# Kernel tuning notes

Hardware: AMD Instinct MI355X
Metric: run time of the kernel (lower is better)

The kernel has to match this reference:

```python
import jax, jax.numpy as jnp
from jax import lax
import numpy as np

N, CIN, COUT, H, W = 8, 64, 64, 256, 256
KH = KW = 3
AUX, HID = 128, 256


def setup_inputs() -> dict:
    key = jax.random.key(0)
    ks = jax.random.split(key, 12)
    k = float(np.sqrt(1.0 / (CIN * KH * KW)))
    inp = {
        "x": jax.random.normal(ks[0], (N, CIN, H, W), jnp.float32),
        "y": jax.random.normal(ks[1], (N, AUX), jnp.float32),
        "weight": jax.random.uniform(ks[2], (COUT, CIN, KH, KW), jnp.float32, -k, k),
        # modulation MLP: Linear(AUX->HID), PReLU, Linear(HID->COUT*CIN), Sigmoid
        "fc_w1": jax.random.normal(ks[3], (HID, AUX), jnp.float32) * 0.05,
        "fc_b1": jax.random.normal(ks[4], (HID,), jnp.float32) * 0.05,
        "fc_prelu": jnp.asarray(0.25, jnp.float32),
        "fc_w2": jax.random.normal(ks[5], (COUT * CIN, HID), jnp.float32) * 0.05,
        "fc_b2": jax.random.normal(ks[6], (COUT * CIN,), jnp.float32) * 0.05,
        # learned-bias MLP: Linear(AUX->HID), PReLU, Linear(HID->COUT)
        "bias_w1": jax.random.normal(ks[7], (HID, AUX), jnp.float32) * 0.05,
        "bias_b1": jax.random.normal(ks[8], (HID,), jnp.float32) * 0.05,
        "bias_prelu": jnp.asarray(0.25, jnp.float32),
        "bias_w2": jax.random.normal(ks[9], (COUT, HID), jnp.float32) * 0.05,
        "bias_b2": jax.random.normal(ks[10], (COUT,), jnp.float32) * 0.05,
    }
    return inp


def _prelu(h, a):
    return jnp.where(h >= 0, h, a * h)


def reference(x, y, weight, fc_w1, fc_b1, fc_prelu, fc_w2, fc_b2,
              bias_w1, bias_b1, bias_prelu, bias_w2, bias_b2):
    n, cin, h_, w_ = x.shape
    cout = weight.shape[0]
    # modulation factors: (N, COUT*CIN), sigmoid activation
    hm = _prelu(y @ fc_w1.T + fc_b1, fc_prelu)
    mod = jax.nn.sigmoid(hm @ fc_w2.T + fc_b2)
    # per-sample modulated kernels: (N, COUT, CIN, KH, KW)
    w_mod = mod.reshape(n, cout, cin, 1, 1) * weight
    # grouped conv with groups = batch, expressed as vmap over batch
    def conv1(xi, wi):  # xi: (CIN,H,W), wi: (COUT,CIN,KH,KW)
        return lax.conv_general_dilated(
            xi[None], wi, window_strides=(1, 1), padding=[(1, 1), (1, 1)],
            rhs_dilation=(1, 1))[0]
    out = jax.vmap(conv1)(x, w_mod)  # (N, COUT, H, W)
    # learned per-sample bias
    hb = _prelu(y @ bias_w1.T + bias_b1, bias_prelu)
    b = hb @ bias_w2.T + bias_b2  # (N, COUT)
    return out + b[:, :, None, None]
```

## Files before the change

kernel.cpp:

```cpp
#include <hip/hip_runtime.h>
#include <hip/hip_bf16.h>


typedef short bf16x8 __attribute__((ext_vector_type(8)));
typedef float f32x16 __attribute__((ext_vector_type(16)));

#define NB 8
#define CIN 64
#define COUT 64
#define HH 256
#define WW 256
#define HWP (HH * WW)
#define AUXD 128
#define HIDD 256

#define XH 4128
#define XRW (2 * XH)
#define XBUF (4 * XRW)
#define WOFF (2 * XBUF)
#define WBYTES (9 * 8 * 64 * 16)
#define SMEMB (WOFF + WBYTES)

__device__ __forceinline__ unsigned short f2bf(float f) {
    unsigned u = __builtin_bit_cast(unsigned, f);
    u += 0x7FFFu + ((u >> 16) & 1u);
    return (unsigned short)(u >> 16);
}

__device__ __forceinline__ unsigned pk2(float a, float b, float vm) {
    return (unsigned)f2bf(a * vm) | ((unsigned)f2bf(b * vm) << 16);
}

__global__ __launch_bounds__(256) void mlp_kernel(
    const float* __restrict__ y, const float* __restrict__ weight,
    const float* __restrict__ fc_w1, const float* __restrict__ fc_b1,
    const float* __restrict__ fc_prelu,
    const float* __restrict__ fc_w2, const float* __restrict__ fc_b2,
    const float* __restrict__ bias_w1, const float* __restrict__ bias_b1,
    const float* __restrict__ bias_prelu,
    const float* __restrict__ bias_w2, const float* __restrict__ bias_b2,
    unsigned short* __restrict__ w_bf, float* __restrict__ bvec)
{
    const int n = blockIdx.y;
    const int c = blockIdx.x;
    const int tid = threadIdx.x;
    __shared__ float ylds[AUXD];
    __shared__ float hl[HIDD];
    if (tid < AUXD) ylds[tid] = y[n * AUXD + tid];
    __syncthreads();

    if (c < 16) {
        float s = fc_b1[tid];
        const float* wrow = fc_w1 + tid * AUXD;
        #pragma unroll 4
        for (int a = 0; a < AUXD; ++a) s += ylds[a] * wrow[a];
        float ap = fc_prelu[0];
        hl[tid] = s >= 0.f ? s : ap * s;
        __syncthreads();

        int o = c * 256 + tid;
        float t = fc_b2[o];
        const float* w2row = fc_w2 + o * HIDD;
        #pragma unroll 4
        for (int h = 0; h < HIDD; ++h) t += hl[h] * w2row[h];
        float mod = 1.f / (1.f + expf(-t));
        int cout = o >> 6, ci = o & 63;
        int cb = ci >> 3, cl = ci & 7;
        #pragma unroll
        for (int k = 0; k < 9; ++k) {
            float wv = weight[o * 9 + k];
            w_bf[((((n * 9 + k) * 8 + cb) * 64 + cout) << 3) + cl] = f2bf(mod * wv);
        }
    } else {
        float s = bias_b1[tid];
        const float* wrow = bias_w1 + tid * AUXD;
        #pragma unroll 4
        for (int a = 0; a < AUXD; ++a) s += ylds[a] * wrow[a];
        float ap = bias_prelu[0];
        hl[tid] = s >= 0.f ? s : ap * s;
        __syncthreads();
        if (tid < COUT) {
            float t = bias_b2[tid];
            const float* w2row = bias_w2 + tid * HIDD;
            #pragma unroll 4
            for (int h = 0; h < HIDD; ++h) t += hl[h] * w2row[h];
            bvec[n * COUT + tid] = t;
        }
    }
}

#define ISSUE(k) { _Pragma("unroll") \
    for (int i = 0; i < 16; ++i) st[i] = xr[k][(size_t)(nci + i) * HWP]; }

#define WRITE(k) { float vm = vmr[k]; \
    unsigned char* dst = nx + (rg + 2 * (k)) * XRW + (sw + 1) * 16; \
    uint4 lo, hi; \
    lo.x = pk2(st[0], st[1], vm);  lo.y = pk2(st[2], st[3], vm); \
    lo.z = pk2(st[4], st[5], vm);  lo.w = pk2(st[6], st[7], vm); \
    hi.x = pk2(st[8], st[9], vm);  hi.y = pk2(st[10], st[11], vm); \
    hi.z = pk2(st[12], st[13], vm); hi.w = pk2(st[14], st[15], vm); \
    *(uint4*)dst = lo; *(uint4*)(dst + XH) = hi; }

__global__ __launch_bounds__(512, 2) void conv_kernel(
    const float* __restrict__ x, const unsigned short* __restrict__ w_bf,
    const float* __restrict__ bvec, float* __restrict__ out)
{
    __shared__ __align__(16) unsigned char smem[SMEMB];

    const int bid = blockIdx.x;
    const int n = bid & 7;
    const int h0 = (bid >> 3) * 2;

    const int tid = threadIdx.x;
    const int lane = tid & 63;
    const int wave = tid >> 6;
    const int wr = wave >> 2;
    const int wq = wave & 3;
    const int l5 = lane >> 5;
    const int l31 = lane & 31;

    const int sw = tid & 255;
    const int rg = tid >> 8;

    const float* xr[2];
    float vmr[2];
    #pragma unroll
    for (int k = 0; k < 2; ++k) {
        int r = rg + 2 * k;
        int hin = h0 - 1 + r;
        bool val = (hin >= 0) && (hin < HH);
        xr[k] = x + (size_t)n * CIN * HWP + (size_t)(val ? hin : 0) * WW + sw;
        vmr[k] = val ? 1.f : 0.f;
    }

    {
        const uint4* wsrc = (const uint4*)w_bf + (size_t)n * (9 * 8 * 64);
        #pragma unroll
        for (int it = 0; it < 9; ++it) {
            int idx = it * 512 + tid;
            uint4 v = wsrc[idx];
            *(uint4*)(smem + WOFF + (idx << 4)) = v;
        }
    }

    if (tid < 32) {
        int buf = tid >> 4, side = (tid >> 3) & 1, r = (tid >> 1) & 3, hf = tid & 1;
        uint4 z; z.x = z.y = z.z = z.w = 0u;
        *(uint4*)(smem + buf * XBUF + r * XRW + hf * XH + (side ? 257 : 0) * 16) = z;
    }

    #pragma unroll
    for (int k = 0; k < 2; ++k) {
        float st[16];
        #pragma unroll
        for (int i = 0; i < 16; ++i) st[i] = xr[k][(size_t)i * HWP];
        float vm = vmr[k];
        unsigned char* dst = smem + (rg + 2 * k) * XRW + (sw + 1) * 16;
        uint4 lo, hi;
        lo.x = pk2(st[0], st[1], vm);  lo.y = pk2(st[2], st[3], vm);
        lo.z = pk2(st[4], st[5], vm);  lo.w = pk2(st[6], st[7], vm);
        hi.x = pk2(st[8], st[9], vm);  hi.y = pk2(st[10], st[11], vm);
        hi.z = pk2(st[12], st[13], vm); hi.w = pk2(st[14], st[15], vm);
        *(uint4*)dst = lo; *(uint4*)(dst + XH) = hi;
    }

    f32x16 acc[2][2];
    #pragma unroll
    for (int m = 0; m < 2; ++m) {
        #pragma unroll
        for (int reg = 0; reg < 16; ++reg)
            acc[m][0][reg] = bvec[n * COUT + m * 32 + (reg & 3) + 8 * (reg >> 2) + 4 * l5];
        acc[m][1] = acc[m][0];
    }

    __syncthreads();

    for (int c = 0; c < 4; ++c) {
        const int p = c & 1;
        const unsigned char* rbuf = smem + p * XBUF;
        unsigned char* nx = smem + (p ^ 1) * XBUF;
        const bool more = (c < 3);
        const int nci = (c + 1) * 16;

        float st[16];
        if (more) ISSUE(0);

        #pragma unroll
        for (int kidx = 0; kidx < 9; ++kidx) {
            const int kh = kidx / 3, kw = kidx % 3;
            const unsigned char* ab = smem + WOFF +
                (((kidx * 8 + c * 2 + l5) * 64 + l31) << 4);
            bf16x8 aA = *(const bf16x8*)ab;
            bf16x8 aB = *(const bf16x8*)(ab + 512);
            const unsigned char* bb = rbuf + (wr + kh) * XRW + l5 * XH;
            bf16x8 b0 = *(const bf16x8*)(bb + (wq * 64 + l31 + kw) * 16);
            bf16x8 b1 = *(const bf16x8*)(bb + (wq * 64 + 32 + l31 + kw) * 16);

            if (more) {
                if (kidx == 3)      { WRITE(0); ISSUE(1); }
                else if (kidx == 7) { WRITE(1); }
            }

            acc[0][0] = __builtin_amdgcn_mfma_f32_32x32x16_bf16(aA, b0, acc[0][0], 0, 0, 0);
            acc[0][1] = __builtin_amdgcn_mfma_f32_32x32x16_bf16(aA, b1, acc[0][1], 0, 0, 0);
            acc[1][0] = __builtin_amdgcn_mfma_f32_32x32x16_bf16(aB, b0, acc[1][0], 0, 0, 0);
            acc[1][1] = __builtin_amdgcn_mfma_f32_32x32x16_bf16(aB, b1, acc[1][1], 0, 0, 0);
        }
        __syncthreads();
    }

    const int hout = h0 + wr;
    float* ob = out + ((size_t)n * COUT * HH + hout) * WW;
    #pragma unroll
    for (int m = 0; m < 2; ++m) {
        #pragma unroll
        for (int j = 0; j < 2; ++j) {
            int colb = wq * 64 + j * 32 + l31;
            #pragma unroll
            for (int reg = 0; reg < 16; ++reg) {
                int cout = m * 32 + (reg & 3) + 8 * (reg >> 2) + 4 * l5;
                ob[(size_t)cout * HWP + colb] = acc[m][j][reg];
            }
        }
    }
}

extern "C" void kernel_launch(void* const* d_in, const int* in_sizes, int n_in,
                              void* d_out, int out_size, void* d_ws, size_t ws_size,
                              hipStream_t stream) {
    const float* x          = (const float*)d_in[0];
    const float* y          = (const float*)d_in[1];
    const float* weight     = (const float*)d_in[2];
    const float* fc_w1      = (const float*)d_in[3];
    const float* fc_b1      = (const float*)d_in[4];
    const float* fc_prelu   = (const float*)d_in[5];
    const float* fc_w2      = (const float*)d_in[6];
    const float* fc_b2      = (const float*)d_in[7];
    const float* bias_w1    = (const float*)d_in[8];
    const float* bias_b1    = (const float*)d_in[9];
    const float* bias_prelu = (const float*)d_in[10];
    const float* bias_w2    = (const float*)d_in[11];
    const float* bias_b2    = (const float*)d_in[12];
    float* out = (float*)d_out;

    unsigned short* w_bf = (unsigned short*)d_ws;
    float* bvec = (float*)((char*)d_ws + (size_t)NB * 9 * 64 * 64 * 2);

    hipLaunchKernelGGL(mlp_kernel, dim3(17, 8), dim3(256), 0, stream,
                       y, weight, fc_w1, fc_b1, fc_prelu, fc_w2, fc_b2,
                       bias_w1, bias_b1, bias_prelu, bias_w2, bias_b2, w_bf, bvec);
    hipLaunchKernelGGL(conv_kernel, dim3(1024), dim3(512), 0, stream,
                       x, w_bf, bvec, out);
}
```

Baseline: 87.65 us.

## Double conv block to 1024 threads with one column tile per wave

Each conv block now runs 16 waves instead of 8. Every wave computes a single 32-column tile instead of two, and every thread stages one input row instead of two. The global-to-LDS prefetch schedule is rewritten so the next channel chunk is written at kidx 6 and the one after is issued at kidx 7. The goal is more waves in flight per CU to hide global-load and LDS latency in this bandwidth-heavy conv, since the large LDS footprint already allows only one block per CU. The cost is that A-operand LDS reads are duplicated across twice as many waves, and each wave does fewer MFMAs per loaded A fragment.

```diff
diff --git a/kernel.cpp b/kernel.cpp
--- a/kernel.cpp
+++ b/kernel.cpp
@@ -89,11 +89,11 @@
     }
 }
 
-#define ISSUE(k) { _Pragma("unroll") \
-    for (int i = 0; i < 16; ++i) st[i] = xr[k][(size_t)(nci + i) * HWP]; }
-
-#define WRITE(k) { float vm = vmr[k]; \
-    unsigned char* dst = nx + (rg + 2 * (k)) * XRW + (sw + 1) * 16; \
+#define ISSUE(ci0) { _Pragma("unroll") \
+    for (int i = 0; i < 16; ++i) st[i] = xrow[(size_t)((ci0) + i) * HWP]; }
+
+#define WRITE(buf) { \
+    unsigned char* dst = (buf) + rg * XRW + (sw + 1) * 16; \
     uint4 lo, hi; \
     lo.x = pk2(st[0], st[1], vm);  lo.y = pk2(st[2], st[3], vm); \
     lo.z = pk2(st[4], st[5], vm);  lo.w = pk2(st[6], st[7], vm); \
@@ -101,7 +101,7 @@
     hi.z = pk2(st[12], st[13], vm); hi.w = pk2(st[14], st[15], vm); \
     *(uint4*)dst = lo; *(uint4*)(dst + XH) = hi; }
 
-__global__ __launch_bounds__(512, 2) void conv_kernel(
+__global__ __launch_bounds__(1024, 4) void conv_kernel(
     const float* __restrict__ x, const unsigned short* __restrict__ w_bf,
     const float* __restrict__ bvec, float* __restrict__ out)
 {
@@ -114,32 +114,28 @@
     const int tid = threadIdx.x;
     const int lane = tid & 63;
     const int wave = tid >> 6;
-    const int wr = wave >> 2;
-    const int wq = wave & 3;
+    const int wr = wave >> 3;
+    const int jt = wave & 7;
     const int l5 = lane >> 5;
     const int l31 = lane & 31;
 
     const int sw = tid & 255;
     const int rg = tid >> 8;
 
-    const float* xr[2];
-    float vmr[2];
-    #pragma unroll
-    for (int k = 0; k < 2; ++k) {
-        int r = rg + 2 * k;
-        int hin = h0 - 1 + r;
-        bool val = (hin >= 0) && (hin < HH);
-        xr[k] = x + (size_t)n * CIN * HWP + (size_t)(val ? hin : 0) * WW + sw;
-        vmr[k] = val ? 1.f : 0.f;
-    }
+    const int hin = h0 - 1 + rg;
+    const bool val = (hin >= 0) && (hin < HH);
+    const float vm = val ? 1.f : 0.f;
+    const float* xrow = x + (size_t)n * CIN * HWP + (size_t)(val ? hin : 0) * WW + sw;
 
     {
         const uint4* wsrc = (const uint4*)w_bf + (size_t)n * (9 * 8 * 64);
         #pragma unroll
-        for (int it = 0; it < 9; ++it) {
-            int idx = it * 512 + tid;
-            uint4 v = wsrc[idx];
-            *(uint4*)(smem + WOFF + (idx << 4)) = v;
+        for (int it = 0; it < 5; ++it) {
+            int idx = it * 1024 + tid;
+            if (idx < 9 * 8 * 64) {
+                uint4 v = wsrc[idx];
+                *(uint4*)(smem + WOFF + (idx << 4)) = v;
+            }
         }
     }
 
@@ -149,29 +145,17 @@
         *(uint4*)(smem + buf * XBUF + r * XRW + hf * XH + (side ? 257 : 0) * 16) = z;
     }
 
+    float st[16];
+    ISSUE(0);
+    WRITE(smem);
+    ISSUE(16);
+
+    f32x16 acc[2];
     #pragma unroll
-    for (int k = 0; k < 2; ++k) {
-        float st[16];
-        #pragma unroll
-        for (int i = 0; i < 16; ++i) st[i] = xr[k][(size_t)i * HWP];
-        float vm = vmr[k];
-        unsigned char* dst = smem + (rg + 2 * k) * XRW + (sw + 1) * 16;
-        uint4 lo, hi;
-        lo.x = pk2(st[0], st[1], vm);  lo.y = pk2(st[2], st[3], vm);
-        lo.z = pk2(st[4], st[5], vm);  lo.w = pk2(st[6], st[7], vm);
-        hi.x = pk2(st[8], st[9], vm);  hi.y = pk2(st[10], st[11], vm);
-        hi.z = pk2(st[12], st[13], vm); hi.w = pk2(st[14], st[15], vm);
-        *(uint4*)dst = lo; *(uint4*)(dst + XH) = hi;
-    }
-
-    f32x16 acc[2][2];
-    #pragma unroll
-    for (int m = 0; m < 2; ++m) {
+    for (int m = 0; m < 2; ++m)
         #pragma unroll
         for (int reg = 0; reg < 16; ++reg)
-            acc[m][0][reg] = bvec[n * COUT + m * 32 + (reg & 3) + 8 * (reg >> 2) + 4 * l5];
-        acc[m][1] = acc[m][0];
-    }
+            acc[m][reg] = bvec[n * COUT + m * 32 + (reg & 3) + 8 * (reg >> 2) + 4 * l5];
 
     __syncthreads();
 
@@ -179,11 +163,6 @@
         const int p = c & 1;
         const unsigned char* rbuf = smem + p * XBUF;
         unsigned char* nx = smem + (p ^ 1) * XBUF;
-        const bool more = (c < 3);
-        const int nci = (c + 1) * 16;
-
-        float st[16];
-        if (more) ISSUE(0);
 
         #pragma unroll
         for (int kidx = 0; kidx < 9; ++kidx) {
@@ -192,35 +171,27 @@
                 (((kidx * 8 + c * 2 + l5) * 64 + l31) << 4);
             bf16x8 aA = *(const bf16x8*)ab;
             bf16x8 aB = *(const bf16x8*)(ab + 512);
-            const unsigned char* bb = rbuf + (wr + kh) * XRW + l5 * XH;
-            bf16x8 b0 = *(const bf16x8*)(bb + (wq * 64 + l31 + kw) * 16);
-            bf16x8 b1 = *(const bf16x8*)(bb + (wq * 64 + 32 + l31 + kw) * 16);
-
-            if (more) {
-                if (kidx == 3)      { WRITE(0); ISSUE(1); }
-                else if (kidx == 7) { WRITE(1); }
-            }
-
-            acc[0][0] = __builtin_amdgcn_mfma_f32_32x32x16_bf16(aA, b0, acc[0][0], 0, 0, 0);
-            acc[0][1] = __builtin_amdgcn_mfma_f32_32x32x16_bf16(aA, b1, acc[0][1], 0, 0, 0);
-            acc[1][0] = __builtin_amdgcn_mfma_f32_32x32x16_bf16(aB, b0, acc[1][0], 0, 0, 0);
-            acc[1][1] = __builtin_amdgcn_mfma_f32_32x32x16_bf16(aB, b1, acc[1][1], 0, 0, 0);
+            bf16x8 b0 = *(const bf16x8*)(rbuf + (wr + kh) * XRW + l5 * XH +
+                                         (jt * 32 + l31 + kw) * 16);
+
+            if (c < 3 && kidx == 6) { WRITE(nx); }
+            if (c < 2 && kidx == 7) { ISSUE((c + 2) * 16); }
+
+            acc[0] = __builtin_amdgcn_mfma_f32_32x32x16_bf16(aA, b0, acc[0], 0, 0, 0);
+            acc[1] = __builtin_amdgcn_mfma_f32_32x32x16_bf16(aB, b0, acc[1], 0, 0, 0);
         }
         __syncthreads();
     }
 
     const int hout = h0 + wr;
     float* ob = out + ((size_t)n * COUT * HH + hout) * WW;
+    const int colb = jt * 32 + l31;
     #pragma unroll
     for (int m = 0; m < 2; ++m) {
         #pragma unroll
-        for (int j = 0; j < 2; ++j) {
-            int colb = wq * 64 + j * 32 + l31;
-            #pragma unroll
-            for (int reg = 0; reg < 16; ++reg) {
-                int cout = m * 32 + (reg & 3) + 8 * (reg >> 2) + 4 * l5;
-                ob[(size_t)cout * HWP + colb] = acc[m][j][reg];
-            }
+        for (int reg = 0; reg < 16; ++reg) {
+            int cout = m * 32 + (reg & 3) + 8 * (reg >> 2) + 4 * l5;
+            ob[(size_t)cout * HWP + colb] = acc[m][reg];
         }
     }
 }
@@ -249,6 +220,6 @@
     hipLaunchKernelGGL(mlp_kernel, dim3(17, 8), dim3(256), 0, stream,
                        y, weight, fc_w1, fc_b1, fc_prelu, fc_w2, fc_b2,
                        bias_w1, bias_b1, bias_prelu, bias_w2, bias_b2, w_bf, bvec);
-    hipLaunchKernelGGL(conv_kernel, dim3(1024), dim3(512), 0, stream,
+    hipLaunchKernelGGL(conv_kernel, dim3(1024), dim3(1024), 0, stream,
                        x, w_bf, bvec, out);
 }
```

Result: slower. 91.48 us (+4.4%).

## Stream weights per 8-channel chunk and pair kernel taps to cut LDS for higher occupancy

Applied to the files above, without the earlier changes.

Stops holding the full per-sample bf16 weight tensor in LDS and instead double-buffers a small weight slot per 8-input-channel chunk. Each MFMA's K=16 is now split across two kernel taps (one per half-wave), with a zero slot padding the odd ninth tap. This shrinks shared memory so launch bounds can go from 2 to 4 blocks per SM and overlaps the weight and input prefetch with compute. In exchange there are twice as many chunk iterations and syncs, five MFMA steps per chunk with one partly wasted on zero padding, and fewer registers per thread.

```diff
diff --git a/kernel.cpp b/kernel.cpp
--- a/kernel.cpp
+++ b/kernel.cpp
@@ -14,12 +14,11 @@
 #define AUXD 128
 #define HIDD 256
 
-#define XH 4128
-#define XRW (2 * XH)
-#define XBUF (4 * XRW)
-#define WOFF (2 * XBUF)
-#define WBYTES (9 * 8 * 64 * 16)
-#define SMEMB (WOFF + WBYTES)
+#define XRW8 (258 * 16)
+#define XBUF (4 * XRW8)
+#define WOFF0 (2 * XBUF)
+#define WSLOT ((9 * 64 + 1) * 16)
+#define SMEMB (WOFF0 + 2 * WSLOT)
 
 __device__ __forceinline__ unsigned short f2bf(float f) {
     unsigned u = __builtin_bit_cast(unsigned, f);
@@ -89,19 +88,22 @@
     }
 }
 
-#define ISSUE(k) { _Pragma("unroll") \
-    for (int i = 0; i < 16; ++i) st[i] = xr[k][(size_t)(nci + i) * HWP]; }
-
-#define WRITE(k) { float vm = vmr[k]; \
-    unsigned char* dst = nx + (rg + 2 * (k)) * XRW + (sw + 1) * 16; \
-    uint4 lo, hi; \
-    lo.x = pk2(st[0], st[1], vm);  lo.y = pk2(st[2], st[3], vm); \
-    lo.z = pk2(st[4], st[5], vm);  lo.w = pk2(st[6], st[7], vm); \
-    hi.x = pk2(st[8], st[9], vm);  hi.y = pk2(st[10], st[11], vm); \
-    hi.z = pk2(st[12], st[13], vm); hi.w = pk2(st[14], st[15], vm); \
-    *(uint4*)dst = lo; *(uint4*)(dst + XH) = hi; }
-
-__global__ __launch_bounds__(512, 2) void conv_kernel(
+#define XISSUE(stv, k, ci0) { _Pragma("unroll") \
+    for (int i = 0; i < 8; ++i) stv[i] = xr[k][(size_t)((ci0) + i) * HWP]; }
+
+#define XWRITE(stv, k, buf) { float vm = vmr[k]; uint4 v; \
+    v.x = pk2(stv[0], stv[1], vm); v.y = pk2(stv[2], stv[3], vm); \
+    v.z = pk2(stv[4], stv[5], vm); v.w = pk2(stv[6], stv[7], vm); \
+    *(uint4*)((buf) + (rg + 2 * (k)) * XRW8 + (sw + 1) * 16) = v; }
+
+#define WLOAD(cc) { wv0 = wsrc[((tid >> 6) << 9) + (cc) * 64 + (tid & 63)]; \
+    if (tid < 64) wv1 = wsrc[4096 + (cc) * 64 + tid]; }
+
+#define WSTORE(pp) { unsigned char* wd = smem + WOFF0 + (pp) * WSLOT; \
+    *(uint4*)(wd + (tid << 4)) = wv0; \
+    if (tid < 64) *(uint4*)(wd + ((512 + tid) << 4)) = wv1; }
+
+__global__ __launch_bounds__(512, 4) void conv_kernel(
     const float* __restrict__ x, const unsigned short* __restrict__ w_bf,
     const float* __restrict__ bvec, float* __restrict__ out)
 {
@@ -133,36 +135,25 @@
         vmr[k] = val ? 1.f : 0.f;
     }
 
-    {
-        const uint4* wsrc = (const uint4*)w_bf + (size_t)n * (9 * 8 * 64);
-        #pragma unroll
-        for (int it = 0; it < 9; ++it) {
-            int idx = it * 512 + tid;
-            uint4 v = wsrc[idx];
-            *(uint4*)(smem + WOFF + (idx << 4)) = v;
-        }
-    }
-
-    if (tid < 32) {
-        int buf = tid >> 4, side = (tid >> 3) & 1, r = (tid >> 1) & 3, hf = tid & 1;
+    const uint4* wsrc = (const uint4*)w_bf + (size_t)n * (9 * 8 * 64);
+    uint4 wv0, wv1;
+
+    if (tid < 16) {
+        int buf = tid >> 3, r = (tid >> 1) & 3, side = tid & 1;
         uint4 z; z.x = z.y = z.z = z.w = 0u;
-        *(uint4*)(smem + buf * XBUF + r * XRW + hf * XH + (side ? 257 : 0) * 16) = z;
-    }
-
-    #pragma unroll
-    for (int k = 0; k < 2; ++k) {
-        float st[16];
-        #pragma unroll
-        for (int i = 0; i < 16; ++i) st[i] = xr[k][(size_t)i * HWP];
-        float vm = vmr[k];
-        unsigned char* dst = smem + (rg + 2 * k) * XRW + (sw + 1) * 16;
-        uint4 lo, hi;
-        lo.x = pk2(st[0], st[1], vm);  lo.y = pk2(st[2], st[3], vm);
-        lo.z = pk2(st[4], st[5], vm);  lo.w = pk2(st[6], st[7], vm);
-        hi.x = pk2(st[8], st[9], vm);  hi.y = pk2(st[10], st[11], vm);
-        hi.z = pk2(st[12], st[13], vm); hi.w = pk2(st[14], st[15], vm);
-        *(uint4*)dst = lo; *(uint4*)(dst + XH) = hi;
-    }
+        *(uint4*)(smem + buf * XBUF + r * XRW8 + (side ? 257 : 0) * 16) = z;
+    }
+    if (tid >= 16 && tid < 18) {
+        uint4 z; z.x = z.y = z.z = z.w = 0u;
+        *(uint4*)(smem + WOFF0 + (tid - 16) * WSLOT + 576 * 16) = z;
+    }
+
+    float stA[8], stB[8];
+    WLOAD(0);
+    XISSUE(stA, 0, 0); XWRITE(stA, 0, smem);
+    XISSUE(stB, 1, 0); XWRITE(stB, 1, smem);
+    WSTORE(0);
+    XISSUE(stA, 0, 8);
 
     f32x16 acc[2][2];
     #pragma unroll
@@ -175,31 +166,37 @@
 
     __syncthreads();
 
-    for (int c = 0; c < 4; ++c) {
+    for (int c = 0; c < 8; ++c) {
         const int p = c & 1;
         const unsigned char* rbuf = smem + p * XBUF;
+        const unsigned char* wb = smem + WOFF0 + p * WSLOT;
         unsigned char* nx = smem + (p ^ 1) * XBUF;
-        const bool more = (c < 3);
-        const int nci = (c + 1) * 16;
-
-        float st[16];
-        if (more) ISSUE(0);
-
-        #pragma unroll
-        for (int kidx = 0; kidx < 9; ++kidx) {
-            const int kh = kidx / 3, kw = kidx % 3;
-            const unsigned char* ab = smem + WOFF +
-                (((kidx * 8 + c * 2 + l5) * 64 + l31) << 4);
-            bf16x8 aA = *(const bf16x8*)ab;
-            bf16x8 aB = *(const bf16x8*)(ab + 512);
-            const unsigned char* bb = rbuf + (wr + kh) * XRW + l5 * XH;
-            bf16x8 b0 = *(const bf16x8*)(bb + (wq * 64 + l31 + kw) * 16);
-            bf16x8 b1 = *(const bf16x8*)(bb + (wq * 64 + 32 + l31 + kw) * 16);
-
-            if (more) {
-                if (kidx == 3)      { WRITE(0); ISSUE(1); }
-                else if (kidx == 7) { WRITE(1); }
-            }
+        const bool more = (c < 7);
+
+        #pragma unroll
+        for (int s = 0; s < 5; ++s) {
+            const int ka = 2 * s;
+            const int kb = (s == 4) ? 8 : 2 * s + 1;
+            const int khA = ka / 3, kwA = ka % 3;
+            const int khB = kb / 3, kwB = kb % 3;
+            const bool solo = (s == 4);
+
+            int au = (solo && l5) ? 576 : ((l5 ? kb : ka) * 64 + l31);
+            int am = (solo && l5) ? 0 : 32;
+            bf16x8 aA = *(const bf16x8*)(wb + (au << 4));
+            bf16x8 aB = *(const bf16x8*)(wb + ((au + am) << 4));
+
+            int kh = l5 ? khB : khA;
+            int kw = l5 ? kwB : kwA;
+            const unsigned char* bb = rbuf + (wr + kh) * XRW8;
+            bf16x8 b0 = *(const bf16x8*)(bb + ((wq * 64 + l31 + kw) << 4));
+            bf16x8 b1 = *(const bf16x8*)(bb + ((wq * 64 + 32 + l31 + kw) << 4));
+
+            if (s == 0 && more) { WLOAD(c + 1); }
+            if (s == 1 && more) { XWRITE(stA, 0, nx); XISSUE(stB, 1, (c + 1) * 8); }
+            if (s == 3 && more) { XWRITE(stB, 1, nx);
+                                  if (c < 6) { XISSUE(stA, 0, (c + 2) * 8); } }
+            if (s == 4 && more) { WSTORE(p ^ 1); }
 
             acc[0][0] = __builtin_amdgcn_mfma_f32_32x32x16_bf16(aA, b0, acc[0][0], 0, 0, 0);
             acc[0][1] = __builtin_amdgcn_mfma_f32_32x32x16_bf16(aA, b1, acc[0][1], 0, 0, 0);
```

Result: slower. 95.85 us (+9.3%).
